# Optimization experiments

Hardware: AMD Instinct MI355X
Metric: run time of the kernel (lower is better)

## Reference

```python
import jax, jax.numpy as jnp
import numpy as np

NUM_HEADS = 8

def setup_inputs() -> dict:
    key = jax.random.key(0)
    k1, k2, k3 = jax.random.split(key, 3)
    query = jax.random.normal(k1, (2, 2048, 512), jnp.float32)   # [B, Tq, out_DIM]
    value = jax.random.normal(k2, (2, 2048, 64), jnp.float32)    # [B, Tv, out_DIM//H]
    conv_w = jax.random.normal(k3, (512, 64, 1), jnp.float32) * 0.05  # Conv1d weight [out, in, 1]
    conv_b = jnp.zeros((512,), jnp.float32)
    return {"query": query, "value": value, "conv_w": conv_w, "conv_b": conv_b}

def reference(query, value, conv_w, conv_b):
    B, Tq, D = query.shape
    H = NUM_HEADS
    dh = D // H  # 64
    # Conv1d with kernel_size=1 over the feature axis == pointwise linear
    k = jnp.einsum('btd,od->bto', value, conv_w[:, :, 0]) + conv_b  # [B, Tv, D]
    Tv = k.shape[1]
    # split heads
    qs = query.reshape(B, Tq, H, dh).transpose(0, 2, 1, 3)  # [B,H,Tq,dh]
    ks = k.reshape(B, Tv, H, dh).transpose(0, 2, 1, 3)      # [B,H,Tv,dh]
    vs = jnp.broadcast_to(value[:, None], (B, H, Tv, dh))   # v repeated per head
    # scaled dot product (normalize=True)
    qk = jnp.einsum('bhqd,bhkd->bhqk', qs, ks) * (dh ** -0.5)  # [B,H,Tq,Tv]
    # F.softmax(qk) with no dim on a 4D tensor uses legacy implicit dim=1 (heads)
    weights = jax.nn.softmax(qk, axis=1)
    ctx = jnp.einsum('bhqk,bhkd->bhqd', weights, vs)  # [B,H,Tq,dh]
    # combine heads
    return ctx.transpose(0, 2, 1, 3).reshape(B, Tq, H * dh)  # [B,Tq,D]
```

## Files before the change

### kernel.cpp

```cpp
#include <hip/hip_runtime.h>
#include <hip/hip_bf16.h>

#define BATCH 2
#define TSEQ  2048
#define DMODEL 512
#define NHEAD 8
#define DHEAD 64

typedef __bf16 bf16x2 __attribute__((ext_vector_type(2)));
typedef __bf16 bf16x4 __attribute__((ext_vector_type(4)));
typedef __bf16 bf16x8 __attribute__((ext_vector_type(8)));
typedef float  f32x4  __attribute__((ext_vector_type(4)));

#if __has_builtin(__builtin_amdgcn_exp2f)
#define EXP2(x) __builtin_amdgcn_exp2f(x)
#else
#define EXP2(x) exp2f(x)
#endif

__device__ __forceinline__ bf16x8 load_b8(const void* p) {
  return __builtin_bit_cast(bf16x8, *reinterpret_cast<const uint4*>(p));
}

__device__ __forceinline__ bf16x8 cvt8(const float* p) {
  float4 a = *reinterpret_cast<const float4*>(p);
  float4 b = *reinterpret_cast<const float4*>(p + 4);
  bf16x8 r;
  r[0] = (__bf16)a.x; r[1] = (__bf16)a.y; r[2] = (__bf16)a.z; r[3] = (__bf16)a.w;
  r[4] = (__bf16)b.x; r[5] = (__bf16)b.y; r[6] = (__bf16)b.z; r[7] = (__bf16)b.w;
  return r;
}

__device__ __forceinline__ bf16x8 cvt8s(const float* p, float s) {
  float4 a = *reinterpret_cast<const float4*>(p);
  float4 b = *reinterpret_cast<const float4*>(p + 4);
  bf16x8 r;
  r[0] = (__bf16)(a.x * s); r[1] = (__bf16)(a.y * s);
  r[2] = (__bf16)(a.z * s); r[3] = (__bf16)(a.w * s);
  r[4] = (__bf16)(b.x * s); r[5] = (__bf16)(b.y * s);
  r[6] = (__bf16)(b.z * s); r[7] = (__bf16)(b.w * s);
  return r;
}

__device__ __forceinline__ uint packbf(float a, float b) {
  uint ua = __builtin_bit_cast(uint, a);
  uint ub = __builtin_bit_cast(uint, b);
  return (ua >> 16) | (ub & 0xFFFF0000u);
}

#define KT_B   1048576
#define KT_T   8192
#define VT_B   131072
#define VT_K   2048

__global__ __launch_bounds__(256) void conv_kernel(
    const float* __restrict__ V,
    const float* __restrict__ W,
    const float* __restrict__ bias,
    __hip_bfloat16* __restrict__ Kt) {
  const int bx = blockIdx.x;
  const int b    = bx >> 7;
  const int tset = bx & 127;
  const int t0   = tset << 4;
  const int w  = threadIdx.x >> 6;
  const int l  = threadIdx.x & 63;
  const int lm = l & 15;
  const int lg = l >> 4;

  const float* vrow = V + ((size_t)(b * TSEQ + t0 + lm)) * DHEAD;
  bf16x8 av0 = cvt8(vrow + lg * 8);
  bf16x8 av1 = cvt8(vrow + 32 + lg * 8);

  #pragma unroll
  for (int n = 0; n < 8; ++n) {
    const int o0 = (w * 8 + n) * 16;
    const float* wrow = W + ((size_t)(o0 + lm)) * DHEAD;
    bf16x8 b0 = cvt8(wrow + lg * 8);
    bf16x8 b1 = cvt8(wrow + 32 + lg * 8);
    f32x4 acc = {0.f, 0.f, 0.f, 0.f};
    acc = __builtin_amdgcn_mfma_f32_16x16x32_bf16(av0, b0, acc, 0, 0, 0);
    acc = __builtin_amdgcn_mfma_f32_16x16x32_bf16(av1, b1, acc, 0, 0, 0);
    const int o   = o0 + lm;
    const int h   = o >> 6;
    const int gg  = (o >> 5) & 1;
    const int lgt = (o >> 3) & 3;
    const int j   = o & 7;
    const float bv = bias[o];
    const size_t kbase = (size_t)b * KT_B + (size_t)tset * KT_T +
                         h * 1024 + gg * 512 + lgt * 128 + j;
    #pragma unroll
    for (int r = 0; r < 4; ++r)
      Kt[kbase + (size_t)(lg * 4 + r) * 8] = __float2bfloat16(acc[r] + bv);
  }
}

__global__ __launch_bounds__(256) void vt_kernel(const float* __restrict__ V,
                                                 __hip_bfloat16* __restrict__ Vtile) {
  const int bx = blockIdx.x;
  const int b  = bx >> 5;
  const int t0 = (bx & 31) << 6;
  const int tid = threadIdx.x;
  __shared__ float tile[64][65];

  #pragma unroll
  for (int p = 0; p < 4; ++p) {
    const int r = p * 16 + (tid >> 4);
    const int c = (tid & 15) * 4;
    float4 v = *reinterpret_cast<const float4*>(
        &V[((size_t)(b * TSEQ + t0 + r)) * DHEAD + c]);
    tile[r][c]     = v.x;
    tile[r][c + 1] = v.y;
    tile[r][c + 2] = v.z;
    tile[r][c + 3] = v.w;
  }
  __syncthreads();

  const int dt = tid >> 6;
  const int l  = tid & 63;
  const int lm = l & 15;
  const int lg = l >> 4;
  #pragma unroll
  for (int ks2 = 0; ks2 < 2; ++ks2) {
    bf16x8 o;
    #pragma unroll
    for (int jj = 0; jj < 4; ++jj) {
      o[jj]     = (__bf16)tile[ks2 * 32 + lg * 4 + jj][dt * 16 + lm];
      o[jj + 4] = (__bf16)tile[ks2 * 32 + 16 + lg * 4 + jj][dt * 16 + lm];
    }
    *reinterpret_cast<uint4*>(
        Vtile + (size_t)b * VT_B + (size_t)((t0 >> 5) + ks2) * VT_K +
        dt * 512 + l * 8) = __builtin_bit_cast(uint4, o);
  }
}

template <int KCH>
__global__ __launch_bounds__(256, 2) void attn_kernel(
    const float* __restrict__ Q,
    const __hip_bfloat16* __restrict__ Kt,
    const __hip_bfloat16* __restrict__ Vtile,
    float* __restrict__ Out,
    __hip_bfloat16* __restrict__ Pp) {
  const int bx = blockIdx.x;
  int b, q0, c;
  if (KCH == 2) {
    const int L = (bx & 7) * 64 + (bx >> 3);
    b = L >> 8; const int rest = L & 255; q0 = (rest >> 1) << 4; c = rest & 1;
  } else {
    const int L = (bx & 7) * 32 + (bx >> 3);
    b = L >> 7; q0 = (L & 127) << 4; c = 0;
  }
  const int tid = threadIdx.x;
  const int w  = tid >> 6;
  const int l  = tid & 63;
  const int lm = l & 15;
  const int lg = l >> 4;

  constexpr int NRND = KCH == 2 ? 8 : 16;
  const int tsbase = c * 64;
  const int kvbase = c * 32;

  __shared__ __bf16 Qs[8192];
  __shared__ __bf16 Ws[4][NHEAD][512];
  __shared__ float  Obuf[64][17];

  const float cl2 = 0.125f * 1.44269504f;
  {
    const int hg = tid >> 4;
    const int wi = tid & 15;
    const int h = hg >> 1, g = hg & 1;
    #pragma unroll
    for (int u = 0; u < 4; ++u) {
      const int ll = u * 16 + wi;
      const float* src = Q + ((size_t)(b * TSEQ + q0 + wi)) * DMODEL +
                         h * DHEAD + g * 32 + u * 8;
      *(bf16x8*)((char*)Qs + hg * 1024 + ll * 16) = cvt8s(src, cl2);
    }
  }
  __syncthreads();

  f32x4 accO[NHEAD];
  #pragma unroll
  for (int h = 0; h < NHEAD; ++h) accO[h] = (f32x4){0.f, 0.f, 0.f, 0.f};

  bf16x8 vA[4], vB[4];

  #define S_HALF(TSET, S2)                                                    \
    {                                                                         \
      const __hip_bfloat16* kb_ =                                             \
          Kt + (size_t)b * KT_B + (size_t)(TSET) * KT_T + l * 8;              \
      bf16x8 kf0[NHEAD], kf1[NHEAD];                                          \
      _Pragma("unroll")                                                       \
      for (int h = 0; h < NHEAD; ++h) {                                       \
        kf0[h] = load_b8(kb_ + h * 1024);                                     \
        kf1[h] = load_b8(kb_ + h * 1024 + 512);                               \
      }                                                                       \
      f32x4 sv[NHEAD];                                                        \
      __builtin_amdgcn_s_setprio(1);                                          \
      _Pragma("unroll")                                                       \
      for (int h = 0; h < NHEAD; ++h) {                                       \
        bf16x8 q0_ = *(const bf16x8*)((const char*)Qs + (h * 2) * 1024 + l * 16);     \
        bf16x8 q1_ = *(const bf16x8*)((const char*)Qs + (h * 2 + 1) * 1024 + l * 16); \
        f32x4 t = {0.f, 0.f, 0.f, 0.f};                                       \
        t = __builtin_amdgcn_mfma_f32_16x16x32_bf16(kf0[h], q0_, t, 0, 0, 0); \
        t = __builtin_amdgcn_mfma_f32_16x16x32_bf16(kf1[h], q1_, t, 0, 0, 0); \
        sv[h] = t;                                                            \
      }                                                                       \
      __builtin_amdgcn_s_setprio(0);                                          \
      _Pragma("unroll")                                                       \
      for (int rp = 0; rp < 2; ++rp) {                                        \
        float w0_[NHEAD], w1_[NHEAD];                                         \
        float s0_ = 0.f, s1_ = 0.f;                                           \
        _Pragma("unroll")                                                     \
        for (int h = 0; h < NHEAD; ++h) { w0_[h] = EXP2(sv[h][2 * rp]);     s0_ += w0_[h]; } \
        _Pragma("unroll")                                                     \
        for (int h = 0; h < NHEAD; ++h) { w1_[h] = EXP2(sv[h][2 * rp + 1]); s1_ += w1_[h]; } \
        const float i0_ = __builtin_amdgcn_rcpf(s0_);                         \
        const float i1_ = __builtin_amdgcn_rcpf(s1_);                         \
        _Pragma("unroll")                                                     \
        for (int h = 0; h < NHEAD; ++h)                                       \
          wfu[h][(S2) * 2 + rp] = packbf(w0_[h] * i0_, w1_[h] * i1_);         \
      }                                                                       \
    }

  #define ROUND(R, VCUR, VNXT)                                                \
    {                                                                         \
      uint wfu[NHEAD][4];                                                     \
      const int ts0 = tsbase + (R) * 8 + w * 2;                               \
      S_HALF(ts0, 0);                                                         \
      S_HALF(ts0 + 1, 1);                                                     \
      _Pragma("unroll")                                                       \
      for (int h = 0; h < NHEAD; ++h)                                         \
        *reinterpret_cast<uint4*>((char*)(&Ws[w][h][0]) + l * 16) =           \
            uint4{wfu[h][0], wfu[h][1], wfu[h][2], wfu[h][3]};                \
      {                                                                       \
        const int RN = (R) < NRND - 1 ? (R) + 1 : NRND - 1;                   \
        const __hip_bfloat16* vb_ = Vtile + (size_t)b * VT_B +                \
            (size_t)(kvbase + RN * 4) * VT_K + w * 512 + l * 8;               \
        _Pragma("unroll")                                                     \
        for (int s = 0; s < 4; ++s) VNXT[s] = load_b8(vb_ + s * 2048);        \
      }                                                                       \
      __syncthreads();                                                        \
      __builtin_amdgcn_s_setprio(1);                                          \
      _Pragma("unroll")                                                       \
      for (int s = 0; s < 4; ++s) {                                           \
        _Pragma("unroll")                                                     \
        for (int h = 0; h < NHEAD; ++h) {                                     \
          bf16x8 wsf = *(const bf16x8*)((const char*)(&Ws[s][h][0]) + l * 16);\
          accO[h] = __builtin_amdgcn_mfma_f32_16x16x32_bf16(VCUR[s], wsf, accO[h], 0, 0, 0); \
        }                                                                     \
      }                                                                       \
      __builtin_amdgcn_s_setprio(0);                                          \
      __syncthreads();                                                        \
    }

  {
    const __hip_bfloat16* vb_ = Vtile + (size_t)b * VT_B +
        (size_t)kvbase * VT_K + w * 512 + l * 8;
    #pragma unroll
    for (int s = 0; s < 4; ++s) vA[s] = load_b8(vb_ + s * 2048);
  }

  #pragma unroll 1
  for (int rp2 = 0; rp2 < NRND / 2; ++rp2) {
    ROUND(2 * rp2,     vA, vB);
    ROUND(2 * rp2 + 1, vB, vA);
  }

  #undef ROUND
  #undef S_HALF

  __hip_bfloat16* pbase = Pp +
      ((size_t)((b * 128 + (q0 >> 4)) * 2 + c)) * 8192;
  float* obase = Out + ((size_t)(b * TSEQ + q0)) * DMODEL;
  #pragma unroll
  for (int h = 0; h < NHEAD; ++h) {
    #pragma unroll
    for (int r = 0; r < 4; ++r)
      Obuf[w * 16 + lg * 4 + r][lm] = accO[h][r];
    __syncthreads();
    {
      const int q  = tid >> 4;
      const int d0 = (tid & 15) * 4;
      float4 s = {Obuf[d0][q], Obuf[d0 + 1][q], Obuf[d0 + 2][q], Obuf[d0 + 3][q]};
      if (KCH == 2) {
        bf16x4 pb;
        pb[0] = (__bf16)s.x; pb[1] = (__bf16)s.y;
        pb[2] = (__bf16)s.z; pb[3] = (__bf16)s.w;
        *reinterpret_cast<uint2*>(&pbase[(size_t)q * 512 + h * DHEAD + d0]) =
            __builtin_bit_cast(uint2, pb);
      } else {
        *reinterpret_cast<float4*>(&obase[(size_t)q * 512 + h * DHEAD + d0]) = s;
      }
    }
    __syncthreads();
  }
}

__global__ void reduce_kernel(const __hip_bfloat16* __restrict__ Pp,
                              float* __restrict__ Out) {
  const int g  = blockIdx.x * 256 + threadIdx.x;
  const int f0 = g << 3;
  const int d0 = f0 & 511;
  const int q  = (f0 >> 9) & 2047;
  const int b  = f0 >> 20;
  const __hip_bfloat16* p = Pp +
      ((size_t)(b * 128 + (q >> 4)) * 2) * 8192 + (size_t)(q & 15) * 512 + d0;
  float acc[8] = {0.f, 0.f, 0.f, 0.f, 0.f, 0.f, 0.f, 0.f};
  #pragma unroll
  for (int c = 0; c < 2; ++c) {
    uint4 u = *reinterpret_cast<const uint4*>(p + c * 8192);
    const uint uu[4] = {u.x, u.y, u.z, u.w};
    #pragma unroll
    for (int j = 0; j < 4; ++j) {
      acc[2 * j]     += __builtin_bit_cast(float, uu[j] << 16);
      acc[2 * j + 1] += __builtin_bit_cast(float, uu[j] & 0xFFFF0000u);
    }
  }
  float4* o = reinterpret_cast<float4*>(Out + f0);
  o[0] = float4{acc[0], acc[1], acc[2], acc[3]};
  o[1] = float4{acc[4], acc[5], acc[6], acc[7]};
}

extern "C" void kernel_launch(void* const* d_in, const int* in_sizes, int n_in,
                              void* d_out, int out_size, void* d_ws, size_t ws_size,
                              hipStream_t stream) {
  const float* Q    = (const float*)d_in[0];
  const float* V    = (const float*)d_in[1];
  const float* W    = (const float*)d_in[2];
  const float* bias = (const float*)d_in[3];
  float* Out = (float*)d_out;

  __hip_bfloat16* Ktb = (__hip_bfloat16*)d_ws;
  __hip_bfloat16* Vtb = Ktb + (size_t)BATCH * KT_B;
  const size_t pOff = 4u * 1024 * 1024 + 512u * 1024;
  __hip_bfloat16* Pp = (__hip_bfloat16*)((char*)d_ws + pOff);
  const bool split = ws_size >= pOff + (size_t)2 * BATCH * TSEQ * DMODEL * 2;

  conv_kernel<<<256, 256, 0, stream>>>(V, W, bias, Ktb);
  vt_kernel<<<64, 256, 0, stream>>>(V, Vtb);
  if (split) {
    attn_kernel<2><<<512, 256, 0, stream>>>(Q, Ktb, Vtb, Out, Pp);
    reduce_kernel<<<1024, 256, 0, stream>>>(Pp, Out);
  } else {
    attn_kernel<1><<<256, 256, 0, stream>>>(Q, Ktb, Vtb, Out, Pp);
  }
}
```

Baseline: 53.05 us.

## Split attention over four key chunks with aliased LDS and higher occupancy

Splits the key/value range into four chunks instead of two, launching 1024 blocks with bf16 partial outputs that the reduce kernel sums over four slices. LDS for Q, weights and the output staging buffer is aliased into one 48KB array, and launch bounds are raised to three blocks per CU. The V double-buffer prefetch is removed in favour of a simple per-round load. The aim is more parallelism and occupancy. The cost is a larger partial buffer, more reduce traffic, extra bf16 rounding of partials, and loss of the V load overlap.

Result: slower. 84.17 us (+58.6%).

```diff
diff --git a/kernel.cpp b/kernel.cpp
--- a/kernel.cpp
+++ b/kernel.cpp
@@ -134,7 +134,7 @@
 }
 
 template <int KCH>
-__global__ __launch_bounds__(256, 2) void attn_kernel(
+__global__ __launch_bounds__(256, 3) void attn_kernel(
     const float* __restrict__ Q,
     const __hip_bfloat16* __restrict__ Kt,
     const __hip_bfloat16* __restrict__ Vtile,
@@ -142,9 +142,9 @@
     __hip_bfloat16* __restrict__ Pp) {
   const int bx = blockIdx.x;
   int b, q0, c;
-  if (KCH == 2) {
-    const int L = (bx & 7) * 64 + (bx >> 3);
-    b = L >> 8; const int rest = L & 255; q0 = (rest >> 1) << 4; c = rest & 1;
+  if (KCH == 4) {
+    const int L = (bx & 7) * 128 + (bx >> 3);
+    b = L >> 9; const int rest = L & 511; q0 = (rest >> 2) << 4; c = rest & 3;
   } else {
     const int L = (bx & 7) * 32 + (bx >> 3);
     b = L >> 7; q0 = (L & 127) << 4; c = 0;
@@ -155,13 +155,14 @@
   const int lm = l & 15;
   const int lg = l >> 4;
 
-  constexpr int NRND = KCH == 2 ? 8 : 16;
-  const int tsbase = c * 64;
-  const int kvbase = c * 32;
-
-  __shared__ __bf16 Qs[8192];
-  __shared__ __bf16 Ws[4][NHEAD][512];
-  __shared__ float  Obuf[64][17];
+  constexpr int NRND = KCH == 4 ? 4 : 16;
+  const int tsbase = c * (128 / KCH);
+  const int kvbase = c * (64 / KCH);
+
+  __shared__ __align__(16) char LdsC[49152];
+  __bf16* Qs = (__bf16*)LdsC;
+  __bf16 (*Ws)[NHEAD][512] = (__bf16 (*)[NHEAD][512])(LdsC + 16384);
+  float (*Obuf)[17] = (float (*)[17])LdsC;
 
   const float cl2 = 0.125f * 1.44269504f;
   {
@@ -181,8 +182,6 @@
   f32x4 accO[NHEAD];
   #pragma unroll
   for (int h = 0; h < NHEAD; ++h) accO[h] = (f32x4){0.f, 0.f, 0.f, 0.f};
-
-  bf16x8 vA[4], vB[4];
 
   #define S_HALF(TSET, S2)                                                    \
     {                                                                         \
@@ -222,55 +221,43 @@
       }                                                                       \
     }
 
-  #define ROUND(R, VCUR, VNXT)                                                \
-    {                                                                         \
-      uint wfu[NHEAD][4];                                                     \
-      const int ts0 = tsbase + (R) * 8 + w * 2;                               \
-      S_HALF(ts0, 0);                                                         \
-      S_HALF(ts0 + 1, 1);                                                     \
-      _Pragma("unroll")                                                       \
-      for (int h = 0; h < NHEAD; ++h)                                         \
-        *reinterpret_cast<uint4*>((char*)(&Ws[w][h][0]) + l * 16) =           \
-            uint4{wfu[h][0], wfu[h][1], wfu[h][2], wfu[h][3]};                \
-      {                                                                       \
-        const int RN = (R) < NRND - 1 ? (R) + 1 : NRND - 1;                   \
-        const __hip_bfloat16* vb_ = Vtile + (size_t)b * VT_B +                \
-            (size_t)(kvbase + RN * 4) * VT_K + w * 512 + l * 8;               \
-        _Pragma("unroll")                                                     \
-        for (int s = 0; s < 4; ++s) VNXT[s] = load_b8(vb_ + s * 2048);        \
-      }                                                                       \
-      __syncthreads();                                                        \
-      __builtin_amdgcn_s_setprio(1);                                          \
-      _Pragma("unroll")                                                       \
-      for (int s = 0; s < 4; ++s) {                                           \
-        _Pragma("unroll")                                                     \
-        for (int h = 0; h < NHEAD; ++h) {                                     \
-          bf16x8 wsf = *(const bf16x8*)((const char*)(&Ws[s][h][0]) + l * 16);\
-          accO[h] = __builtin_amdgcn_mfma_f32_16x16x32_bf16(VCUR[s], wsf, accO[h], 0, 0, 0); \
-        }                                                                     \
-      }                                                                       \
-      __builtin_amdgcn_s_setprio(0);                                          \
-      __syncthreads();                                                        \
-    }
-
-  {
-    const __hip_bfloat16* vb_ = Vtile + (size_t)b * VT_B +
-        (size_t)kvbase * VT_K + w * 512 + l * 8;
-    #pragma unroll
-    for (int s = 0; s < 4; ++s) vA[s] = load_b8(vb_ + s * 2048);
-  }
-
   #pragma unroll 1
-  for (int rp2 = 0; rp2 < NRND / 2; ++rp2) {
-    ROUND(2 * rp2,     vA, vB);
-    ROUND(2 * rp2 + 1, vB, vA);
-  }
-
-  #undef ROUND
+  for (int R = 0; R < NRND; ++R) {
+    bf16x8 vc[4];
+    {
+      const __hip_bfloat16* vb_ = Vtile + (size_t)b * VT_B +
+          (size_t)(kvbase + R * 4) * VT_K + w * 512 + l * 8;
+      #pragma unroll
+      for (int s = 0; s < 4; ++s) vc[s] = load_b8(vb_ + s * VT_K);
+    }
+
+    uint wfu[NHEAD][4];
+    const int ts0 = tsbase + R * 8 + w * 2;
+    S_HALF(ts0, 0);
+    S_HALF(ts0 + 1, 1);
+    #pragma unroll
+    for (int h = 0; h < NHEAD; ++h)
+      *reinterpret_cast<uint4*>((char*)(&Ws[w][h][0]) + l * 16) =
+          uint4{wfu[h][0], wfu[h][1], wfu[h][2], wfu[h][3]};
+    __syncthreads();
+
+    __builtin_amdgcn_s_setprio(1);
+    #pragma unroll
+    for (int s = 0; s < 4; ++s) {
+      #pragma unroll
+      for (int h = 0; h < NHEAD; ++h) {
+        bf16x8 wsf = *(const bf16x8*)((const char*)(&Ws[s][h][0]) + l * 16);
+        accO[h] = __builtin_amdgcn_mfma_f32_16x16x32_bf16(vc[s], wsf, accO[h], 0, 0, 0);
+      }
+    }
+    __builtin_amdgcn_s_setprio(0);
+    __syncthreads();
+  }
+
   #undef S_HALF
 
   __hip_bfloat16* pbase = Pp +
-      ((size_t)((b * 128 + (q0 >> 4)) * 2 + c)) * 8192;
+      ((size_t)((b * 128 + (q0 >> 4)) * 4 + c)) * 8192;
   float* obase = Out + ((size_t)(b * TSEQ + q0)) * DMODEL;
   #pragma unroll
   for (int h = 0; h < NHEAD; ++h) {
@@ -282,7 +269,7 @@
       const int q  = tid >> 4;
       const int d0 = (tid & 15) * 4;
       float4 s = {Obuf[d0][q], Obuf[d0 + 1][q], Obuf[d0 + 2][q], Obuf[d0 + 3][q]};
-      if (KCH == 2) {
+      if (KCH == 4) {
         bf16x4 pb;
         pb[0] = (__bf16)s.x; pb[1] = (__bf16)s.y;
         pb[2] = (__bf16)s.z; pb[3] = (__bf16)s.w;
@@ -304,10 +291,10 @@
   const int q  = (f0 >> 9) & 2047;
   const int b  = f0 >> 20;
   const __hip_bfloat16* p = Pp +
-      ((size_t)(b * 128 + (q >> 4)) * 2) * 8192 + (size_t)(q & 15) * 512 + d0;
+      ((size_t)(b * 128 + (q >> 4)) * 4) * 8192 + (size_t)(q & 15) * 512 + d0;
   float acc[8] = {0.f, 0.f, 0.f, 0.f, 0.f, 0.f, 0.f, 0.f};
   #pragma unroll
-  for (int c = 0; c < 2; ++c) {
+  for (int c = 0; c < 4; ++c) {
     uint4 u = *reinterpret_cast<const uint4*>(p + c * 8192);
     const uint uu[4] = {u.x, u.y, u.z, u.w};
     #pragma unroll
@@ -334,12 +321,12 @@
   __hip_bfloat16* Vtb = Ktb + (size_t)BATCH * KT_B;
   const size_t pOff = 4u * 1024 * 1024 + 512u * 1024;
   __hip_bfloat16* Pp = (__hip_bfloat16*)((char*)d_ws + pOff);
-  const bool split = ws_size >= pOff + (size_t)2 * BATCH * TSEQ * DMODEL * 2;
+  const bool split = ws_size >= pOff + (size_t)4 * BATCH * TSEQ * DMODEL * 2;
 
   conv_kernel<<<256, 256, 0, stream>>>(V, W, bias, Ktb);
   vt_kernel<<<64, 256, 0, stream>>>(V, Vtb);
   if (split) {
-    attn_kernel<2><<<512, 256, 0, stream>>>(Q, Ktb, Vtb, Out, Pp);
+    attn_kernel<4><<<1024, 256, 0, stream>>>(Q, Ktb, Vtb, Out, Pp);
     reduce_kernel<<<1024, 256, 0, stream>>>(Pp, Out);
   } else {
     attn_kernel<1><<<256, 256, 0, stream>>>(Q, Ktb, Vtb, Out, Pp);
```

## Keep Q in registers, double-buffer weight LDS, drop per-round trailing barrier

Applied to the files above, without the earlier changes.

Q fragments are now converted straight into registers per lane instead of being staged through shared memory, which removes the initial barrier and the per-head LDS reads. The softmax-weight buffer is double-buffered by round parity within one aliased 64KB LDS block, so the second __syncthreads per round can go. K fragment loads are moved inside the per-head MFMA loop to cut register pressure from the extra Q registers. The cost is more VGPRs, larger LDS use that may lower occupancy, and K load latency that may now be exposed.

Measured after the change: 63.50 us. 1.2x slower.

```diff
diff --git a/kernel.cpp b/kernel.cpp
--- a/kernel.cpp
+++ b/kernel.cpp
@@ -159,24 +159,20 @@
   const int tsbase = c * 64;
   const int kvbase = c * 32;
 
-  __shared__ __bf16 Qs[8192];
-  __shared__ __bf16 Ws[4][NHEAD][512];
-  __shared__ float  Obuf[64][17];
+  __shared__ __align__(16) char LdsC[65536];
+  __bf16 (*Ws)[4][NHEAD][512] = (__bf16 (*)[4][NHEAD][512])LdsC;
+  float (*Obuf)[17] = (float (*)[17])LdsC;
 
   const float cl2 = 0.125f * 1.44269504f;
+  bf16x8 qf[NHEAD][2];
   {
-    const int hg = tid >> 4;
-    const int wi = tid & 15;
-    const int h = hg >> 1, g = hg & 1;
-    #pragma unroll
-    for (int u = 0; u < 4; ++u) {
-      const int ll = u * 16 + wi;
-      const float* src = Q + ((size_t)(b * TSEQ + q0 + wi)) * DMODEL +
-                         h * DHEAD + g * 32 + u * 8;
-      *(bf16x8*)((char*)Qs + hg * 1024 + ll * 16) = cvt8s(src, cl2);
-    }
-  }
-  __syncthreads();
+    const float* qrow = Q + ((size_t)(b * TSEQ + q0 + lm)) * DMODEL + lg * 8;
+    #pragma unroll
+    for (int h = 0; h < NHEAD; ++h) {
+      qf[h][0] = cvt8s(qrow + h * DHEAD, cl2);
+      qf[h][1] = cvt8s(qrow + h * DHEAD + 32, cl2);
+    }
+  }
 
   f32x4 accO[NHEAD];
   #pragma unroll
@@ -188,21 +184,15 @@
     {                                                                         \
       const __hip_bfloat16* kb_ =                                             \
           Kt + (size_t)b * KT_B + (size_t)(TSET) * KT_T + l * 8;              \
-      bf16x8 kf0[NHEAD], kf1[NHEAD];                                          \
-      _Pragma("unroll")                                                       \
-      for (int h = 0; h < NHEAD; ++h) {                                       \
-        kf0[h] = load_b8(kb_ + h * 1024);                                     \
-        kf1[h] = load_b8(kb_ + h * 1024 + 512);                               \
-      }                                                                       \
       f32x4 sv[NHEAD];                                                        \
       __builtin_amdgcn_s_setprio(1);                                          \
       _Pragma("unroll")                                                       \
       for (int h = 0; h < NHEAD; ++h) {                                       \
-        bf16x8 q0_ = *(const bf16x8*)((const char*)Qs + (h * 2) * 1024 + l * 16);     \
-        bf16x8 q1_ = *(const bf16x8*)((const char*)Qs + (h * 2 + 1) * 1024 + l * 16); \
+        bf16x8 kf0 = load_b8(kb_ + h * 1024);                                 \
+        bf16x8 kf1 = load_b8(kb_ + h * 1024 + 512);                           \
         f32x4 t = {0.f, 0.f, 0.f, 0.f};                                       \
-        t = __builtin_amdgcn_mfma_f32_16x16x32_bf16(kf0[h], q0_, t, 0, 0, 0); \
-        t = __builtin_amdgcn_mfma_f32_16x16x32_bf16(kf1[h], q1_, t, 0, 0, 0); \
+        t = __builtin_amdgcn_mfma_f32_16x16x32_bf16(kf0, qf[h][0], t, 0, 0, 0); \
+        t = __builtin_amdgcn_mfma_f32_16x16x32_bf16(kf1, qf[h][1], t, 0, 0, 0); \
         sv[h] = t;                                                            \
       }                                                                       \
       __builtin_amdgcn_s_setprio(0);                                          \
@@ -222,53 +212,53 @@
       }                                                                       \
     }
 
-  #define ROUND(R, VCUR, VNXT)                                                \
-    {                                                                         \
-      uint wfu[NHEAD][4];                                                     \
-      const int ts0 = tsbase + (R) * 8 + w * 2;                               \
-      S_HALF(ts0, 0);                                                         \
-      S_HALF(ts0 + 1, 1);                                                     \
-      _Pragma("unroll")                                                       \
-      for (int h = 0; h < NHEAD; ++h)                                         \
-        *reinterpret_cast<uint4*>((char*)(&Ws[w][h][0]) + l * 16) =           \
-            uint4{wfu[h][0], wfu[h][1], wfu[h][2], wfu[h][3]};                \
-      {                                                                       \
-        const int RN = (R) < NRND - 1 ? (R) + 1 : NRND - 1;                   \
-        const __hip_bfloat16* vb_ = Vtile + (size_t)b * VT_B +                \
-            (size_t)(kvbase + RN * 4) * VT_K + w * 512 + l * 8;               \
-        _Pragma("unroll")                                                     \
-        for (int s = 0; s < 4; ++s) VNXT[s] = load_b8(vb_ + s * 2048);        \
-      }                                                                       \
-      __syncthreads();                                                        \
-      __builtin_amdgcn_s_setprio(1);                                          \
-      _Pragma("unroll")                                                       \
-      for (int s = 0; s < 4; ++s) {                                           \
-        _Pragma("unroll")                                                     \
-        for (int h = 0; h < NHEAD; ++h) {                                     \
-          bf16x8 wsf = *(const bf16x8*)((const char*)(&Ws[s][h][0]) + l * 16);\
+  #define ROUND(R, P, VCUR, VNXT)                                            \
+    {                                                                        \
+      uint wfu[NHEAD][4];                                                    \
+      const int ts0 = tsbase + (R) * 8 + w * 2;                              \
+      S_HALF(ts0, 0);                                                        \
+      S_HALF(ts0 + 1, 1);                                                    \
+      _Pragma("unroll")                                                      \
+      for (int h = 0; h < NHEAD; ++h)                                        \
+        *reinterpret_cast<uint4*>((char*)(&Ws[P][w][h][0]) + l * 16) =       \
+            uint4{wfu[h][0], wfu[h][1], wfu[h][2], wfu[h][3]};               \
+      {                                                                      \
+        const int RN = (R) < NRND - 1 ? (R) + 1 : NRND - 1;                  \
+        const __hip_bfloat16* vb_ = Vtile + (size_t)b * VT_B +               \
+            (size_t)(kvbase + RN * 4) * VT_K + w * 512 + l * 8;              \
+        _Pragma("unroll")                                                    \
+        for (int s = 0; s < 4; ++s) VNXT[s] = load_b8(vb_ + s * VT_K);       \
+      }                                                                      \
+      __syncthreads();                                                       \
+      __builtin_amdgcn_s_setprio(1);                                         \
+      _Pragma("unroll")                                                      \
+      for (int s = 0; s < 4; ++s) {                                          \
+        _Pragma("unroll")                                                    \
+        for (int h = 0; h < NHEAD; ++h) {                                    \
+          bf16x8 wsf = *(const bf16x8*)((const char*)(&Ws[P][s][h][0]) + l * 16); \
           accO[h] = __builtin_amdgcn_mfma_f32_16x16x32_bf16(VCUR[s], wsf, accO[h], 0, 0, 0); \
-        }                                                                     \
-      }                                                                       \
-      __builtin_amdgcn_s_setprio(0);                                          \
-      __syncthreads();                                                        \
+        }                                                                    \
+      }                                                                      \
+      __builtin_amdgcn_s_setprio(0);                                         \
     }
 
   {
     const __hip_bfloat16* vb_ = Vtile + (size_t)b * VT_B +
         (size_t)kvbase * VT_K + w * 512 + l * 8;
     #pragma unroll
-    for (int s = 0; s < 4; ++s) vA[s] = load_b8(vb_ + s * 2048);
+    for (int s = 0; s < 4; ++s) vA[s] = load_b8(vb_ + s * VT_K);
   }
 
   #pragma unroll 1
   for (int rp2 = 0; rp2 < NRND / 2; ++rp2) {
-    ROUND(2 * rp2,     vA, vB);
-    ROUND(2 * rp2 + 1, vB, vA);
+    ROUND(2 * rp2,     0, vA, vB);
+    ROUND(2 * rp2 + 1, 1, vB, vA);
   }
 
   #undef ROUND
   #undef S_HALF
 
+  __syncthreads();
   __hip_bfloat16* pbase = Pp +
       ((size_t)((b * 128 + (q0 >> 4)) * 2 + c)) * 8192;
   float* obase = Out + ((size_t)(b * TSEQ + q0)) * DMODEL;
```
